# Kernel optimization log

Measured on AMD Instinct MI355X. Metric: run time of the kernel, lower is better.

The kernel has to match this reference:

```python
import jax, jax.numpy as jnp
import numpy as np

# Architecture constants (match init_kwargs)
A = 4            # num_areas
E_PER = 512      # excitatory units per area
I_PER = 128      # inhibitory units per area
H = A * (E_PER + I_PER)   # 2560 hidden units, order: [all E (area-major), all I]
NUM_OBJS = 2
IN_UNITS = 64
IN = NUM_OBJS * IN_UNITS  # 128 input units
DT, TAU_X = 0.02, 0.1
ALPHA_X = DT / TAU_X


def _build_masks():
    """Signed Dale's-law connectivity masks, as in _get_connectivity_mask_* ."""
    # inter-area recurrent connectivity: nearest-neighbor hierarchy + self
    rec = np.eye(A) + np.eye(A, k=1) + np.eye(A, k=-1)
    ee = np.kron(rec, np.ones((E_PER, E_PER)))
    ei = np.kron(np.eye(A), np.ones((E_PER, I_PER)))   # E<-I only within area
    ie = np.kron(rec, np.ones((I_PER, E_PER)))
    ii = np.kron(np.eye(A), np.ones((I_PER, I_PER)))
    conn = np.block([[ee, ei], [ie, ii]])
    # sign mask: first e_size columns excitatory (+1), rest inhibitory (-1)
    sign = np.concatenate([np.ones(A * E_PER), -np.ones(A * I_PER)])[None, :]
    rec_mask = conn * sign
    np.fill_diagonal(rec_mask, 0.0)  # remove_diag=True in h2h EILinear
    # input mask: only area 0 receives external input; e_prop=1 for x2h (all +1)
    in_area = np.zeros((A, NUM_OBJS)); in_area[0, :] = 1.0
    in_e = np.kron(in_area, np.ones((E_PER, IN_UNITS)))
    in_i = np.kron(in_area, np.ones((I_PER, IN_UNITS)))
    in_mask = np.concatenate([in_e, in_i], axis=0)
    return jnp.asarray(rec_mask, jnp.float32), jnp.asarray(in_mask, jnp.float32)


def setup_inputs() -> dict:
    key = jax.random.key(0)
    k1, k2, k3 = jax.random.split(key, 3)
    T, B = 500, 64
    inputs = jax.random.normal(k1, (T, B, IN), dtype=jnp.float32)
    W_rec = jax.random.normal(k2, (H, H), dtype=jnp.float32) / np.sqrt(H)
    b_rec = jnp.zeros((H,), dtype=jnp.float32)
    W_in = jax.random.normal(k3, (H, IN), dtype=jnp.float32) / np.sqrt(IN)
    return {"inputs": inputs, "W_rec": W_rec, "b_rec": b_rec, "W_in": W_in}


def reference(inputs, W_rec, b_rec, W_in):
    rec_mask, in_mask = _build_masks()
    # EILinear effective weights: pos_func=abs, times signed connectivity mask
    W_rec_eff = jnp.abs(W_rec) * rec_mask          # [H, H]
    W_in_eff = jnp.abs(W_in) * in_mask             # [H, IN]
    # input projection for all timesteps at once
    proj = jnp.einsum('tbi,hi->tbh', inputs, W_in_eff)  # [T, B, H]

    def retanh(x):
        return jnp.tanh(jax.nn.relu(x))

    def step(carry, u_t):
        x, r = carry
        pre = r @ W_rec_eff.T + b_rec + u_t        # h2h(r) + x2h(u)
        x = (1.0 - ALPHA_X) * x + ALPHA_X * pre    # leaky integration
        r = retanh(x)
        return (x, r), r

    B = inputs.shape[1]
    x0 = jnp.zeros((B, H), dtype=inputs.dtype)     # x0 (train_init_state=False)
    (_, _), rates = jax.lax.scan(step, (x0, retanh(x0)), proj)
    return rates  # [T, B, H] firing rates
```

## Files before the change

### kernel.cpp

```cpp
#include <hip/hip_runtime.h>
#include <math.h>

#define Hn   2560
#define Bn   64
#define INW  128
#define ETOT 2048
#define HGn  160
#define MAXC 13
#define NBLK 160
#define MAXI 7

typedef __attribute__((ext_vector_type(8))) _Float16 half8;
typedef __attribute__((ext_vector_type(4))) float  floatx4;

__global__ void build_apack(const float* __restrict__ Wrec,
                            const float* __restrict__ Win,
                            _Float16* __restrict__ Af) {
  int hg = blockIdx.x, c = blockIdx.y;
  int a = (hg < 128) ? (hg >> 5) : ((hg - 128) >> 3);
  int nE = (a == 0 || a == 3) ? 8 : 12;
  int nch = nE + 1 + (a == 0 ? 1 : 0);
  if (c >= nch) return;
  int h0 = hg * 16;
  int tid = threadIdx.x;
  int kq = tid >> 6, L = tid & 63;
  int m = L & 15, q = L >> 4;
  int h = h0 + m;

  const float* src; int k0, stride; float sgn; bool isIn = false;
  if (c < nE)       { k0 = ((a == 0 ? 0 : a - 1) << 9) + (c << 7); src = Wrec; stride = Hn;  sgn =  1.f; }
  else if (c == nE) { k0 = ETOT + (a << 7);                        src = Wrec; stride = Hn;  sgn = -1.f; }
  else              { k0 = 0;                                      src = Win;  stride = INW; sgn =  1.f; isIn = true; }

  _Float16 hi8[8], lo8[8];
  #pragma unroll
  for (int j = 0; j < 8; ++j) {
    int k = k0 + kq * 32 + q * 8 + j;
    float w = fabsf(src[(size_t)h * stride + k]);
    if (!isIn && k == h) w = 0.f;
    w *= sgn;
    _Float16 wh = (_Float16)w;
    hi8[j] = wh;
    lo8[j] = (_Float16)(w - (float)wh);
  }
  _Float16* outp = Af + (size_t)(hg * MAXC + c) * 4096;
  *(uint4*)(outp + (kq * 2 + 0) * 512 + L * 8) = *(const uint4*)hi8;
  *(uint4*)(outp + (kq * 2 + 1) * 512 + L * 8) = *(const uint4*)lo8;
}

#define LOAD4(B0,B1,B2,B3,P) \
  asm volatile("global_load_dwordx4 %0, %4, off sc0 sc1\n\t" \
               "global_load_dwordx4 %1, %4, off offset:1024 sc0 sc1\n\t" \
               "global_load_dwordx4 %2, %4, off offset:2048 sc0 sc1\n\t" \
               "global_load_dwordx4 %3, %4, off offset:3072 sc0 sc1\n\t" \
               "s_waitcnt vmcnt(0)" \
               : "=&v"(B0), "=&v"(B1), "=&v"(B2), "=&v"(B3) \
               : "v"(P) : "memory")

#define LOAD8(X0,X1,X2,X3,Y0,Y1,Y2,Y3,PA,PB) \
  asm volatile("global_load_dwordx4 %0, %8, off sc0 sc1\n\t" \
               "global_load_dwordx4 %1, %8, off offset:1024 sc0 sc1\n\t" \
               "global_load_dwordx4 %2, %8, off offset:2048 sc0 sc1\n\t" \
               "global_load_dwordx4 %3, %8, off offset:3072 sc0 sc1\n\t" \
               "global_load_dwordx4 %4, %9, off sc0 sc1\n\t" \
               "global_load_dwordx4 %5, %9, off offset:1024 sc0 sc1\n\t" \
               "global_load_dwordx4 %6, %9, off offset:2048 sc0 sc1\n\t" \
               "global_load_dwordx4 %7, %9, off offset:3072 sc0 sc1\n\t" \
               "s_waitcnt vmcnt(0)" \
               : "=&v"(X0), "=&v"(X1), "=&v"(X2), "=&v"(X3), \
                 "=&v"(Y0), "=&v"(Y1), "=&v"(Y2), "=&v"(Y3) \
               : "v"(PA), "v"(PB) : "memory")

#define MFMA8(i, B0,B1,B2,B3) do { \
  ac0 = __builtin_amdgcn_mfma_f32_16x16x32_f16(ah[i], B0, ac0, 0, 0, 0); \
  ac0 = __builtin_amdgcn_mfma_f32_16x16x32_f16(al[i], B0, ac0, 0, 0, 0); \
  ac1 = __builtin_amdgcn_mfma_f32_16x16x32_f16(ah[i], B1, ac1, 0, 0, 0); \
  ac1 = __builtin_amdgcn_mfma_f32_16x16x32_f16(al[i], B1, ac1, 0, 0, 0); \
  ac2 = __builtin_amdgcn_mfma_f32_16x16x32_f16(ah[i], B2, ac2, 0, 0, 0); \
  ac2 = __builtin_amdgcn_mfma_f32_16x16x32_f16(al[i], B2, ac2, 0, 0, 0); \
  ac3 = __builtin_amdgcn_mfma_f32_16x16x32_f16(ah[i], B3, ac3, 0, 0, 0); \
  ac3 = __builtin_amdgcn_mfma_f32_16x16x32_f16(al[i], B3, ac3, 0, 0, 0); \
} while (0)

#define RECPATH1(i) do { \
  half8 B0_, B1_, B2_, B3_; \
  const _Float16* pp_ = rs + boff[i]; \
  LOAD4(B0_, B1_, B2_, B3_, pp_); \
  MFMA8(i, B0_, B1_, B2_, B3_); \
} while (0)

#define INPATH(i) do { \
  const float* ip_ = inputs + (size_t)t * (Bn * INW) + boff[i]; \
  int nb_ = L & 15; \
  half8 B0_, B1_, B2_, B3_; \
  _Pragma("unroll") for (int j = 0; j < 8; ++j) B0_[j] = (_Float16)ip_[(nb_ +  0) * INW + j]; \
  _Pragma("unroll") for (int j = 0; j < 8; ++j) B1_[j] = (_Float16)ip_[(nb_ + 16) * INW + j]; \
  _Pragma("unroll") for (int j = 0; j < 8; ++j) B2_[j] = (_Float16)ip_[(nb_ + 32) * INW + j]; \
  _Pragma("unroll") for (int j = 0; j < 8; ++j) B3_[j] = (_Float16)ip_[(nb_ + 48) * INW + j]; \
  MFMA8(i, B0_, B1_, B2_, B3_); \
} while (0)

#define PAIR(i0, i1) do { \
  bool r0_ = act[i0] && !isin[i0]; \
  bool r1_ = act[i1] && !isin[i1]; \
  if (r0_ && r1_) { \
    half8 X0_,X1_,X2_,X3_,Y0_,Y1_,Y2_,Y3_; \
    const _Float16* pa_ = rs + boff[i0]; \
    const _Float16* pb_ = rs + boff[i1]; \
    LOAD8(X0_,X1_,X2_,X3_,Y0_,Y1_,Y2_,Y3_, pa_, pb_); \
    MFMA8(i0, X0_, X1_, X2_, X3_); \
    MFMA8(i1, Y0_, Y1_, Y2_, Y3_); \
  } else { \
    if (r0_) RECPATH1(i0); else if (act[i0]) INPATH(i0); \
    if (r1_) RECPATH1(i1); else if (act[i1]) INPATH(i1); \
  } \
} while (0)

__global__ __launch_bounds__(512, 2) void rnn_persist(
    const _Float16* __restrict__ Af,
    const float* __restrict__ inputs,
    _Float16* __restrict__ rfA, _Float16* __restrict__ rfB,
    const float* __restrict__ brec,
    float* __restrict__ rates,
    unsigned* bar, int T)
{
  __shared__ float red[8][1056];
  __shared__ float rrt[16][68];
  __shared__ float bb[16];

  const int hg  = blockIdx.x;
  const int tid = threadIdx.x;
  const int w   = tid >> 6, L = tid & 63;
  const int h0  = hg * 16;
  const int a   = (hg < 128) ? (hg >> 5) : ((hg - 128) >> 3);
  const int nE  = (a == 0 || a == 3) ? 8 : 12;
  const int SK  = (nE + 1 + (a == 0 ? 1 : 0)) * 4;
  const int ktE0 = (a == 0 ? 0 : a - 1) * 16;
  const int ktI0 = 64 + a * 4;

  unsigned* bsub = bar + (hg & 7) * 64;
  unsigned* bmas = bar + 8 * 64;
  unsigned* bgen = bar + (9 + (hg & 7)) * 64;

  if (tid < 16) bb[tid] = brec[h0 + tid];

  half8 ah[MAXI], al[MAXI];
  int   boff[MAXI];
  bool  act[MAXI], isin[MAXI];
  const _Float16* Abase = Af + (size_t)hg * MAXC * 4096;
  #pragma unroll
  for (int i = 0; i < MAXI; ++i) {
    half8 zz = {0,0,0,0,0,0,0,0};
    ah[i] = zz; al[i] = zz;
    int ks = w + i * 8;
    act[i]  = ks < SK;
    isin[i] = false;
    boff[i] = 0;
    if (act[i]) {
      int c = ks >> 2, kq = ks & 3;
      const _Float16* Ap = Abase + (size_t)c * 4096 + (size_t)(kq * 2) * 512 + (size_t)L * 8;
      ah[i] = *(const half8*)Ap;
      al[i] = *(const half8*)(Ap + 512);
      if (c <= nE) {
        int kt = (c < nE) ? (ktE0 + c * 4 + kq) : (ktI0 + kq);
        boff[i] = kt * 2048 + L * 8;
      } else {
        isin[i] = true;
        boff[i] = kq * 32 + (L >> 4) * 8;
      }
    }
  }
  #pragma unroll
  for (int i = 0; i < MAXI; ++i)
    asm volatile("" : "+v"(ah[i]), "+v"(al[i]));

  float xv[2] = {0.f, 0.f};

  __syncthreads();

  for (int t = 0; t < T; ++t) {
    const _Float16* __restrict__ rs = (t & 1) ? rfB : rfA;
    _Float16* __restrict__ rd       = (t & 1) ? rfA : rfB;

    floatx4 ac0 = {0.f,0.f,0.f,0.f}, ac1 = {0.f,0.f,0.f,0.f};
    floatx4 ac2 = {0.f,0.f,0.f,0.f}, ac3 = {0.f,0.f,0.f,0.f};

    PAIR(0, 1);
    PAIR(2, 3);
    PAIR(4, 5);
    if (act[6]) { if (!isin[6]) RECPATH1(6); else INPATH(6); }

    #pragma unroll
    for (int p = 0; p < 4; ++p) {
      int m = (L >> 4) * 4 + p;
      float* rw = &red[w][m * 66 + (L & 15)];
      rw[ 0] = ac0[p];
      rw[16] = ac1[p];
      rw[32] = ac2[p];
      rw[48] = ac3[p];
    }
    __syncthreads();

    #pragma unroll
    for (int e = 0; e < 2; ++e) {
      int elem = tid + e * 512;
      int m = elem >> 6, n = elem & 63;
      float s = 0.f;
      #pragma unroll
      for (int j = 0; j < 8; ++j) s += red[j][m * 66 + n];
      float x = 0.8f * xv[e] + 0.2f * (s + bb[m]);
      xv[e] = x;
      float xr = fmaxf(x, 0.f);
      float e2 = __builtin_amdgcn_exp2f(xr * 2.885390081777926814f);
      rrt[m][n] = 1.0f - 2.0f * __builtin_amdgcn_rcpf(e2 + 1.0f);
    }
    __syncthreads();

    if (tid < 128) {
      int bt = tid >> 5, Lq = tid & 31;
      int Lp = (hg & 1) * 32 + Lq;
      half8 vv;
      #pragma unroll
      for (int j = 0; j < 8; ++j)
        vv[j] = (_Float16)rrt[(Lq >> 4) * 8 + j][bt * 16 + (Lq & 15)];
      _Float16* dst = rd + (size_t)((hg >> 1) * 4 + bt) * 512 + (size_t)Lp * 8;
      asm volatile("global_store_dwordx4 %0, %1, off sc0 sc1\n\t"
                   "s_waitcnt vmcnt(0)"
                   :: "v"(dst), "v"(vv) : "memory");
    }
    __syncthreads();

    unsigned g = (unsigned)(t + 1);
    if (t + 1 < T && tid == 0) {
      unsigned s = __hip_atomic_fetch_add(bsub, 1u, __ATOMIC_RELAXED,
                                          __HIP_MEMORY_SCOPE_AGENT);
      if (s == g * 20u - 1u) {
        unsigned m2 = __hip_atomic_fetch_add(bmas, 1u, __ATOMIC_RELAXED,
                                             __HIP_MEMORY_SCOPE_AGENT);
        if (m2 == g * 8u - 1u) {
          #pragma unroll
          for (int x = 0; x < 8; ++x)
            __hip_atomic_store(bar + (9 + x) * 64, g, __ATOMIC_RELAXED,
                               __HIP_MEMORY_SCOPE_AGENT);
        }
      }
    }

    if (tid >= 256) {
      int tt = tid - 256;
      int b = tt >> 2, hq = tt & 3;
      floatx4 o;
      o.x = rrt[hq * 4 + 0][b];
      o.y = rrt[hq * 4 + 1][b];
      o.z = rrt[hq * 4 + 2][b];
      o.w = rrt[hq * 4 + 3][b];
      __builtin_nontemporal_store(o,
          (floatx4*)(rates + (size_t)t * (Bn * Hn) + (size_t)b * Hn + h0 + hq * 4));
    }

    if (t + 1 < T) {
      if (tid == 0) {
        while (__hip_atomic_load(bgen, __ATOMIC_RELAXED,
                                 __HIP_MEMORY_SCOPE_AGENT) < g)
          __builtin_amdgcn_s_sleep(2);
      }
      __syncthreads();
    }
  }
}

extern "C" void kernel_launch(void* const* d_in, const int* in_sizes, int n_in,
                              void* d_out, int out_size, void* d_ws, size_t ws_size,
                              hipStream_t stream) {
  const float* inputs = (const float*)d_in[0];
  const float* Wrec   = (const float*)d_in[1];
  const float* brec   = (const float*)d_in[2];
  const float* Win    = (const float*)d_in[3];
  int T = in_sizes[0] / (Bn * INW);

  char* base = (char*)d_ws;
  size_t off = 0;
  _Float16* Af  = (_Float16*)(base + off); off += (size_t)HGn * MAXC * 4096 * 2;
  _Float16* rfA = (_Float16*)(base + off); off += (size_t)80 * 4 * 512 * 2;
  _Float16* rfB = (_Float16*)(base + off); off += (size_t)80 * 4 * 512 * 2;
  unsigned* bar = (unsigned*)(base + off); off += 8192;

  (void)hipMemsetAsync(rfA, 0, (size_t)80 * 4 * 512 * 2, stream);
  (void)hipMemsetAsync(bar, 0, 8192, stream);

  build_apack<<<dim3(HGn, MAXC), 256, 0, stream>>>(Wrec, Win, Af);

  float* rates = (float*)d_out;
  rnn_persist<<<NBLK, 512, 0, stream>>>(Af, inputs, rfA, rfB, brec, rates,
                                        bar, T);
}
```

Baseline: 2.796 ms.

## Use per-timestep rate buffers and area-interleaved block mapping in persistent RNN

When the workspace is large enough, each timestep writes its rates into a fresh slot instead of ping-ponging between two buffers. Fresh slots avoid stale-cache and write-after-read hazards and could allow looser synchronization. Blocks are remapped so that blocks of the same area are spread across the launch order, likely to balance XCD placement. The inner loop is simplified to a single per-chunk load/MFMA loop, and launch bounds go from 2 to 1 blocks per CU. The trade-offs are a much larger workspace footprint and possibly less load overlap than the paired path.

Result: faster. 2.701 ms (-3.4%).

```diff
diff --git a/kernel.cpp b/kernel.cpp
--- a/kernel.cpp
+++ b/kernel.cpp
@@ -9,6 +9,7 @@
 #define MAXC 13
 #define NBLK 160
 #define MAXI 7
+#define RFSTRIDE (80 * 4 * 512)
 
 typedef __attribute__((ext_vector_type(8))) _Float16 half8;
 typedef __attribute__((ext_vector_type(4))) float  floatx4;
@@ -116,10 +117,11 @@
   } \
 } while (0)
 
-__global__ __launch_bounds__(512, 2) void rnn_persist(
+template <int ROT>
+__global__ __launch_bounds__(512, ROT ? 1 : 2) void rnn_persist(
     const _Float16* __restrict__ Af,
     const float* __restrict__ inputs,
-    _Float16* __restrict__ rfA, _Float16* __restrict__ rfB,
+    _Float16* __restrict__ rfbase,
     const float* __restrict__ brec,
     float* __restrict__ rates,
     unsigned* bar, int T)
@@ -128,7 +130,15 @@
   __shared__ float rrt[16][68];
   __shared__ float bb[16];
 
-  const int hg  = blockIdx.x;
+  const int bid = blockIdx.x;
+  int hg_;
+  if (ROT) {
+    int x = bid & 7, aa = x >> 1, idx = (x & 1) * 20 + (bid >> 3);
+    hg_ = (idx < 32) ? (aa * 32 + idx) : (128 + aa * 8 + (idx - 32));
+  } else {
+    hg_ = bid;
+  }
+  const int hg  = hg_;
   const int tid = threadIdx.x;
   const int w   = tid >> 6, L = tid & 63;
   const int h0  = hg * 16;
@@ -179,16 +189,50 @@
   __syncthreads();
 
   for (int t = 0; t < T; ++t) {
-    const _Float16* __restrict__ rs = (t & 1) ? rfB : rfA;
-    _Float16* __restrict__ rd       = (t & 1) ? rfA : rfB;
+    const _Float16* __restrict__ rs;
+    _Float16* __restrict__ rd;
+    if (ROT) {
+      rs = rfbase + (size_t)t * RFSTRIDE;
+      rd = rfbase + (size_t)(t + 1) * RFSTRIDE;
+    } else {
+      rs = (t & 1) ? (rfbase + RFSTRIDE) : rfbase;
+      rd = (t & 1) ? rfbase : (rfbase + RFSTRIDE);
+    }
 
     floatx4 ac0 = {0.f,0.f,0.f,0.f}, ac1 = {0.f,0.f,0.f,0.f};
     floatx4 ac2 = {0.f,0.f,0.f,0.f}, ac3 = {0.f,0.f,0.f,0.f};
 
-    PAIR(0, 1);
-    PAIR(2, 3);
-    PAIR(4, 5);
-    if (act[6]) { if (!isin[6]) RECPATH1(6); else INPATH(6); }
+    if (ROT) {
+      #pragma unroll
+      for (int i = 0; i < MAXI; ++i) {
+        if (!act[i]) continue;
+        half8 b0, b1, b2, b3;
+        if (isin[i]) {
+          const float* ip = inputs + (size_t)t * (Bn * INW) + boff[i];
+          int nb = L & 15;
+          #pragma unroll
+          for (int j = 0; j < 8; ++j) b0[j] = (_Float16)ip[(nb +  0) * INW + j];
+          #pragma unroll
+          for (int j = 0; j < 8; ++j) b1[j] = (_Float16)ip[(nb + 16) * INW + j];
+          #pragma unroll
+          for (int j = 0; j < 8; ++j) b2[j] = (_Float16)ip[(nb + 32) * INW + j];
+          #pragma unroll
+          for (int j = 0; j < 8; ++j) b3[j] = (_Float16)ip[(nb + 48) * INW + j];
+        } else {
+          const _Float16* Bp = rs + boff[i];
+          b0 = *(const half8*)(Bp);
+          b1 = *(const half8*)(Bp + 512);
+          b2 = *(const half8*)(Bp + 1024);
+          b3 = *(const half8*)(Bp + 1536);
+        }
+        MFMA8(i, b0, b1, b2, b3);
+      }
+    } else {
+      PAIR(0, 1);
+      PAIR(2, 3);
+      PAIR(4, 5);
+      if (act[6]) { if (!isin[6]) RECPATH1(6); else INPATH(6); }
+    }
 
     #pragma unroll
     for (int p = 0; p < 4; ++p) {
@@ -278,19 +322,27 @@
   const float* Win    = (const float*)d_in[3];
   int T = in_sizes[0] / (Bn * INW);
 
+  const size_t afBytes  = (size_t)HGn * MAXC * 4096 * 2;
+  const size_t slotB    = (size_t)RFSTRIDE * 2;
+  const size_t rotBytes = (size_t)(T + 1) * slotB;
+  const size_t barBytes = 8192;
+
   char* base = (char*)d_ws;
-  size_t off = 0;
-  _Float16* Af  = (_Float16*)(base + off); off += (size_t)HGn * MAXC * 4096 * 2;
-  _Float16* rfA = (_Float16*)(base + off); off += (size_t)80 * 4 * 512 * 2;
-  _Float16* rfB = (_Float16*)(base + off); off += (size_t)80 * 4 * 512 * 2;
-  unsigned* bar = (unsigned*)(base + off); off += 8192;
-
-  (void)hipMemsetAsync(rfA, 0, (size_t)80 * 4 * 512 * 2, stream);
-  (void)hipMemsetAsync(bar, 0, 8192, stream);
+  _Float16* Af = (_Float16*)base;
+  _Float16* rf = (_Float16*)(base + afBytes);
+
+  const bool rot = ws_size >= afBytes + rotBytes + barBytes + (1u << 20);
+  const size_t rfBytes = rot ? rotBytes : 2 * slotB;
+  unsigned* bar = (unsigned*)(base + afBytes + rfBytes);
+
+  (void)hipMemsetAsync(rf, 0, slotB, stream);
+  (void)hipMemsetAsync(bar, 0, barBytes, stream);
 
   build_apack<<<dim3(HGn, MAXC), 256, 0, stream>>>(Wrec, Win, Af);
 
   float* rates = (float*)d_out;
-  rnn_persist<<<NBLK, 512, 0, stream>>>(Af, inputs, rfA, rfB, brec, rates,
-                                        bar, T);
+  if (rot)
+    rnn_persist<1><<<NBLK, 512, 0, stream>>>(Af, inputs, rf, brec, rates, bar, T);
+  else
+    rnn_persist<0><<<NBLK, 512, 0, stream>>>(Af, inputs, rf, brec, rates, bar, T);
 }
```
